# Optimization experiments

Hardware: AMD Instinct MI355X
Metric: run time of the kernel (lower is better)

Reference implementation:

```python
import jax, jax.numpy as jnp
import numpy as np

N_SI, N_M, N_INT, E = 100000, 100000, 500000, 500000
D_SI, D_M, D_INT, H1, H2 = 128, 128, 64, 32, 16


def _seg_mean(x_src, src, dst, n_dst):
    # gather src features per edge, scatter-mean into dst nodes
    msg = x_src[src]                                                  # [E, d]
    s = jax.ops.segment_sum(msg, dst, num_segments=n_dst)             # [n_dst, d]
    cnt = jax.ops.segment_sum(jnp.ones((src.shape[0],), x_src.dtype), dst,
                              num_segments=n_dst)
    return s / jnp.maximum(cnt, 1.0)[:, None]


def _sage(x_src, x_dst, src, dst, Wl, Wr, b):
    # PyG SAGEConv: lin_l(mean_aggr) + lin_r(x_dst); bias lives in lin_l
    return _seg_mean(x_src, src, dst, x_dst.shape[0]) @ Wl + b + x_dst @ Wr


def setup_inputs() -> dict:
    key = jax.random.key(0)
    ks = jax.random.split(key, 40)
    f = lambda i, shape: jax.random.normal(ks[i], shape, dtype=jnp.float32)
    w = lambda i, shape: 0.1 * jax.random.normal(ks[i], shape, dtype=jnp.float32)
    inp = {
        'x_si': f(0, (N_SI, D_SI)),
        'x_m': f(1, (N_M, D_M)),
        'x_int': f(2, (N_INT, D_INT)),
        # layer 1 SAGEConv params per relation (Wl: src->out, Wr: dst->out)
        'W1l_si2i': w(3, (D_SI, H1)), 'W1r_si2i': w(4, (D_INT, H1)), 'b1_si2i': w(5, (H1,)),
        'W1l_m2i': w(6, (D_M, H1)), 'W1r_m2i': w(7, (D_INT, H1)), 'b1_m2i': w(8, (H1,)),
        'W1l_si': w(9, (D_SI, H1)), 'W1r_si': w(10, (D_SI, H1)), 'b1_si': w(11, (H1,)),
        'W1l_m': w(12, (D_M, H1)), 'W1r_m': w(13, (D_M, H1)), 'b1_m': w(14, (H1,)),
        # layer 2
        'W2l_si2i': w(15, (H1, H2)), 'W2r_si2i': w(16, (H1, H2)), 'b2_si2i': w(17, (H2,)),
        'W2l_m2i': w(18, (H1, H2)), 'W2r_m2i': w(19, (H1, H2)), 'b2_m2i': w(20, (H2,)),
        'W2l_si': w(21, (H1, H2)), 'W2r_si': w(22, (H1, H2)), 'b2_si': w(23, (H2,)),
        'W2l_m': w(24, (H1, H2)), 'W2r_m': w(25, (H1, H2)), 'b2_m': w(26, (H2,)),
        # final linear
        'Wlin': w(27, (H2, 1)), 'blin': w(28, (1,)),
        # edge lists
        'src_si2i': jax.random.randint(ks[29], (E,), 0, N_SI, dtype=jnp.int32),
        'dst_si2i': jax.random.randint(ks[30], (E,), 0, N_INT, dtype=jnp.int32),
        'src_m2i': jax.random.randint(ks[31], (E,), 0, N_M, dtype=jnp.int32),
        'dst_m2i': jax.random.randint(ks[32], (E,), 0, N_INT, dtype=jnp.int32),
        'sl_si': jnp.arange(N_SI, dtype=jnp.int32),
        'sl_m': jnp.arange(N_M, dtype=jnp.int32),
    }
    return inp


def reference(x_si, x_m, x_int,
              W1l_si2i, W1r_si2i, b1_si2i, W1l_m2i, W1r_m2i, b1_m2i,
              W1l_si, W1r_si, b1_si, W1l_m, W1r_m, b1_m,
              W2l_si2i, W2r_si2i, b2_si2i, W2l_m2i, W2r_m2i, b2_m2i,
              W2l_si, W2r_si, b2_si, W2l_m, W2r_m, b2_m,
              Wlin, blin,
              src_si2i, dst_si2i, src_m2i, dst_m2i, sl_si, sl_m):
    # ---- HeteroConv layer 1 (aggr='mean' across relations per dst type) ----
    h_int = 0.5 * (_sage(x_si, x_int, src_si2i, dst_si2i, W1l_si2i, W1r_si2i, b1_si2i)
                   + _sage(x_m, x_int, src_m2i, dst_m2i, W1l_m2i, W1r_m2i, b1_m2i))
    h_si = _sage(x_si, x_si, sl_si, sl_si, W1l_si, W1r_si, b1_si)
    h_m = _sage(x_m, x_m, sl_m, sl_m, W1l_m, W1r_m, b1_m)
    # ReLU; dropout is identity in eval mode
    h_int, h_si, h_m = jax.nn.relu(h_int), jax.nn.relu(h_si), jax.nn.relu(h_m)
    # ---- HeteroConv layer 2 ----
    h_int2 = 0.5 * (_sage(h_si, h_int, src_si2i, dst_si2i, W2l_si2i, W2r_si2i, b2_si2i)
                    + _sage(h_m, h_int, src_m2i, dst_m2i, W2l_m2i, W2r_m2i, b2_m2i))
    # ---- readout on interaction nodes ----
    return (h_int2 @ Wlin + blin)[:, 0]
```

## Files before the change

kernel.cpp:

```cpp
#include <hip/hip_runtime.h>
#include <cstdint>

#define NSI   100000
#define NM    100000
#define NINT  500000
#define NEDGE 500000
#define NB_SCAN 489

static const long OFF_WSI  = 0;
static const long OFF_WM   = 8192;
static const long OFF_WI   = 16384;
static const long OFF_USI  = 18432;
static const long OFF_UM   = 18464;
static const long OFF_V    = 18496;
static const long OFF_C0   = 18528;
static const long OFF_BI   = 18560;
static const long OFF_PSI  = 18592;
static const long OFF_HSI  = OFF_PSI + 3200000;
static const long OFF_PM   = OFF_HSI + 3200000;
static const long OFF_HM   = OFF_PM + 3200000;
static const long OFF_SSI  = OFF_HM + 3200000;
static const long OFF_SM   = OFF_SSI + 100000;
static const long OFF_RI   = OFF_SM + 100000;
static const long OFF_DEG  = OFF_RI + 16000000;
static const long OFF_RP   = OFF_DEG + 2000000;
static const long OFF_EI   = OFF_RP + 1000000;
static const long OFF_BS   = OFF_EI + 1000000;
static const long OFF_END  = OFF_BS + 1024;

__global__ __launch_bounds__(256) void prep_kernel(
    const float* __restrict__ W1l_si2i, const float* __restrict__ W1l_si, const float* __restrict__ W1r_si,
    const float* __restrict__ W1l_m2i,  const float* __restrict__ W1l_m,  const float* __restrict__ W1r_m,
    const float* __restrict__ W1r_si2i, const float* __restrict__ W1r_m2i,
    const float* __restrict__ b1_si2i,  const float* __restrict__ b1_m2i,
    const float* __restrict__ W2l_si2i, const float* __restrict__ W2l_m2i,
    const float* __restrict__ W2r_si2i, const float* __restrict__ W2r_m2i,
    const float* __restrict__ b2_si2i,  const float* __restrict__ b2_m2i,
    const float* __restrict__ Wlin,     const float* __restrict__ blin,
    float* __restrict__ Wsi, float* __restrict__ Wm, float* __restrict__ Wi, float* __restrict__ bi,
    float* __restrict__ u_si, float* __restrict__ u_m, float* __restrict__ v, float* __restrict__ c0)
{
    const int tid = threadIdx.x;
    for (int idx = tid; idx < 128 * 64; idx += 256) {
        int k = idx >> 6, c = idx & 63;
        float a, b;
        if (c < 32) { a = W1l_si2i[k * 32 + c];      b = W1l_m2i[k * 32 + c]; }
        else { int cc = c - 32;
               a = W1l_si[k * 32 + cc] + W1r_si[k * 32 + cc];
               b = W1l_m[k * 32 + cc]  + W1r_m[k * 32 + cc]; }
        Wsi[idx] = a; Wm[idx] = b;
    }
    for (int idx = tid; idx < 64 * 32; idx += 256)
        Wi[idx] = 0.5f * (W1r_si2i[idx] + W1r_m2i[idx]);
    if (tid < 32) {
        bi[tid] = 0.5f * (b1_si2i[tid] + b1_m2i[tid]);
        float us = 0.f, um = 0.f, vv = 0.f;
        for (int k = 0; k < 16; ++k) {
            float wl = Wlin[k];
            us += W2l_si2i[tid * 16 + k] * wl;
            um += W2l_m2i[tid * 16 + k] * wl;
            vv += 0.5f * (W2r_si2i[tid * 16 + k] + W2r_m2i[tid * 16 + k]) * wl;
        }
        u_si[tid] = us; u_m[tid] = um; v[tid] = vv;
    }
    if (tid == 0) {
        float c = blin[0];
        for (int k = 0; k < 16; ++k) c += 0.5f * (b2_si2i[k] + b2_m2i[k]) * Wlin[k];
        c0[0] = c;
    }
}

__global__ __launch_bounds__(256) void gemm_src(
    const float* __restrict__ X, const float* __restrict__ Wcat, const float* __restrict__ bias,
    float* __restrict__ P, float* __restrict__ H, int N)
{
    __shared__ float xs[64 * 132];
    __shared__ float lw[64 * 64];
    const int tid = threadIdx.x;
    const long row_base = (long)blockIdx.x * 64;

    #pragma unroll
    for (int i = 0; i < 8; ++i) {
        int idx = tid + i * 256;
        int r = idx >> 5, k4 = idx & 31;
        long rr = row_base + r;
        float4 val = make_float4(0.f, 0.f, 0.f, 0.f);
        if (rr < N) val = ((const float4*)X)[rr * 32 + k4];
        *(float4*)&xs[r * 132 + k4 * 4] = val;
    }

    const int r0 = tid & 15;
    const int c0 = (tid >> 4) * 4;
    float acc[4][4] = {{0.f}};

    for (int half = 0; half < 2; ++half) {
        __syncthreads();
        #pragma unroll
        for (int i = 0; i < 4; ++i) {
            int idx = tid + i * 256;
            ((float4*)lw)[idx] = ((const float4*)Wcat)[half * 1024 + idx];
        }
        __syncthreads();
        const float* xb = xs + half * 64;
        #pragma unroll 4
        for (int k = 0; k < 64; k += 4) {
            float4 xr[4];
            #pragma unroll
            for (int j = 0; j < 4; ++j)
                xr[j] = *(const float4*)&xb[(r0 + 16 * j) * 132 + k];
            #pragma unroll
            for (int kk = 0; kk < 4; ++kk) {
                float4 wv = *(const float4*)&lw[(k + kk) * 64 + c0];
                #pragma unroll
                for (int j = 0; j < 4; ++j) {
                    float xv = (kk == 0) ? xr[j].x : (kk == 1) ? xr[j].y : (kk == 2) ? xr[j].z : xr[j].w;
                    acc[j][0] = fmaf(xv, wv.x, acc[j][0]);
                    acc[j][1] = fmaf(xv, wv.y, acc[j][1]);
                    acc[j][2] = fmaf(xv, wv.z, acc[j][2]);
                    acc[j][3] = fmaf(xv, wv.w, acc[j][3]);
                }
            }
        }
    }

    #pragma unroll
    for (int j = 0; j < 4; ++j) {
        long rr = row_base + r0 + 16 * j;
        if (rr >= N) continue;
        if (c0 < 32) {
            *(float4*)&P[rr * 32 + c0] = make_float4(acc[j][0], acc[j][1], acc[j][2], acc[j][3]);
        } else {
            const int cc = c0 - 32;
            float4 o;
            o.x = fmaxf(acc[j][0] + bias[cc + 0], 0.f);
            o.y = fmaxf(acc[j][1] + bias[cc + 1], 0.f);
            o.z = fmaxf(acc[j][2] + bias[cc + 2], 0.f);
            o.w = fmaxf(acc[j][3] + bias[cc + 3], 0.f);
            *(float4*)&H[rr * 32 + cc] = o;
        }
    }
}

__global__ __launch_bounds__(128) void gemm_int(
    const float* __restrict__ X, const float* __restrict__ W,
    const float* __restrict__ bi,
    float* __restrict__ R, int N)
{
    __shared__ float xs[64 * 68];
    __shared__ float lw[64 * 32];
    const int tid = threadIdx.x;
    const long row_base = (long)blockIdx.x * 64;

    #pragma unroll
    for (int i = 0; i < 4; ++i)
        ((float4*)lw)[tid + i * 128] = ((const float4*)W)[tid + i * 128];
    #pragma unroll
    for (int i = 0; i < 8; ++i) {
        int idx = tid + i * 128;
        int r = idx >> 4, k4 = idx & 15;
        long rr = row_base + r;
        float4 val = make_float4(0.f, 0.f, 0.f, 0.f);
        if (rr < N) val = ((const float4*)X)[rr * 16 + k4];
        *(float4*)&xs[r * 68 + k4 * 4] = val;
    }
    __syncthreads();

    const int r0 = tid & 15;
    const int c0 = (tid >> 4) * 4;
    float acc[4][4] = {{0.f}};
    #pragma unroll 4
    for (int k = 0; k < 64; k += 4) {
        float4 xr[4];
        #pragma unroll
        for (int j = 0; j < 4; ++j)
            xr[j] = *(const float4*)&xs[(r0 + 16 * j) * 68 + k];
        #pragma unroll
        for (int kk = 0; kk < 4; ++kk) {
            float4 wv = *(const float4*)&lw[(k + kk) * 32 + c0];
            #pragma unroll
            for (int j = 0; j < 4; ++j) {
                float xv = (kk == 0) ? xr[j].x : (kk == 1) ? xr[j].y : (kk == 2) ? xr[j].z : xr[j].w;
                acc[j][0] = fmaf(xv, wv.x, acc[j][0]);
                acc[j][1] = fmaf(xv, wv.y, acc[j][1]);
                acc[j][2] = fmaf(xv, wv.z, acc[j][2]);
                acc[j][3] = fmaf(xv, wv.w, acc[j][3]);
            }
        }
    }
    #pragma unroll
    for (int j = 0; j < 4; ++j) {
        long rr = row_base + r0 + 16 * j;
        if (rr >= N) continue;
        float4 o;
        o.x = acc[j][0] + bi[c0 + 0];
        o.y = acc[j][1] + bi[c0 + 1];
        o.z = acc[j][2] + bi[c0 + 2];
        o.w = acc[j][3] + bi[c0 + 3];
        *(float4*)&R[rr * 32 + c0] = o;
    }
}

__global__ __launch_bounds__(256) void s_kernel(
    const float* __restrict__ h_si, const float* __restrict__ h_m,
    const float* __restrict__ u_si, const float* __restrict__ u_m,
    float* __restrict__ s_si, float* __restrict__ s_m)
{
    long gid = (long)blockIdx.x * 256 + threadIdx.x;
    long node = gid >> 5;
    int f = (int)(gid & 31);
    if (node >= (long)(NSI + NM)) return;
    const float* h; const float* u; float* s; long n;
    if (node < NSI) { h = h_si; u = u_si; s = s_si; n = node; }
    else            { h = h_m;  u = u_m;  s = s_m;  n = node - NSI; }
    float t = h[n * 32 + f] * u[f];
    #pragma unroll
    for (int off = 16; off > 0; off >>= 1) t += __shfl_xor(t, off);
    if (f == 0) s[n] = t;
}

__global__ __launch_bounds__(256) void hist_kernel(
    const int* __restrict__ dst_si, const int* __restrict__ dst_m,
    int* __restrict__ deg_si, int* __restrict__ deg_m)
{
    int e = blockIdx.x * 256 + threadIdx.x;
    if (e >= NEDGE) return;
    if (blockIdx.y == 0) atomicAdd(&deg_si[dst_si[e]], 1);
    else                 atomicAdd(&deg_m[dst_m[e]], 1);
}

__global__ __launch_bounds__(256) void scan1_kernel(
    const int* __restrict__ deg_si, const int* __restrict__ deg_m,
    int* __restrict__ rp_si, int* __restrict__ rp_m, int* __restrict__ bsum)
{
    const int rel = blockIdx.y;
    const int* deg = rel ? deg_m : deg_si;
    int* rp = rel ? rp_m : rp_si;
    __shared__ int ls[256];
    const int tid = threadIdx.x;
    const int base = blockIdx.x * 1024 + tid * 4;
    int v[4];
    #pragma unroll
    for (int j = 0; j < 4; ++j) v[j] = (base + j < NINT) ? deg[base + j] : 0;
    int tsum = v[0] + v[1] + v[2] + v[3];
    ls[tid] = tsum;
    __syncthreads();
    for (int off = 1; off < 256; off <<= 1) {
        int t = (tid >= off) ? ls[tid - off] : 0;
        __syncthreads();
        ls[tid] += t;
        __syncthreads();
    }
    int run = ls[tid] - tsum;
    #pragma unroll
    for (int j = 0; j < 4; ++j) {
        if (base + j < NINT) rp[base + j] = run;
        run += v[j];
    }
    if (tid == 255) bsum[rel * 512 + blockIdx.x] = ls[255];
}

__global__ __launch_bounds__(512) void scan2_kernel(int* __restrict__ bsum)
{
    int* bs = bsum + blockIdx.y * 512;
    __shared__ int ls[512];
    const int tid = threadIdx.x;
    int v = (tid < NB_SCAN) ? bs[tid] : 0;
    ls[tid] = v;
    __syncthreads();
    for (int off = 1; off < 512; off <<= 1) {
        int t = (tid >= off) ? ls[tid - off] : 0;
        __syncthreads();
        ls[tid] += t;
        __syncthreads();
    }
    bs[tid] = ls[tid] - v;
}

__global__ __launch_bounds__(256) void scan3_kernel(
    int* __restrict__ rp_si, int* __restrict__ rp_m, const int* __restrict__ bsum)
{
    int i = blockIdx.x * 256 + threadIdx.x;
    if (i >= NINT) return;
    int rel = blockIdx.y;
    int* rp = rel ? rp_m : rp_si;
    rp[i] += bsum[rel * 512 + (i >> 10)];
}

__global__ __launch_bounds__(256) void fill_kernel(
    const int* __restrict__ src_si, const int* __restrict__ dst_si,
    const int* __restrict__ src_m,  const int* __restrict__ dst_m,
    const int* __restrict__ rp_si,  const int* __restrict__ rp_m,
    int* __restrict__ cur_si, int* __restrict__ cur_m,
    int* __restrict__ ei_si,  int* __restrict__ ei_m)
{
    int e = blockIdx.x * 256 + threadIdx.x;
    if (e >= NEDGE) return;
    if (blockIdx.y == 0) {
        int dn = dst_si[e], sn = src_si[e];
        int pos = atomicAdd(&cur_si[dn], 1);
        ei_si[rp_si[dn] + pos] = sn;
    } else {
        int dn = dst_m[e], sn = src_m[e];
        int pos = atomicAdd(&cur_m[dn], 1);
        ei_m[rp_m[dn] + pos] = sn;
    }
}

__global__ __launch_bounds__(256) void final_gather(
    const float* __restrict__ r_int,
    const float* __restrict__ p_si, const float* __restrict__ p_m,
    const float* __restrict__ s_si, const float* __restrict__ s_m,
    const int* __restrict__ rp_si, const int* __restrict__ deg_si, const int* __restrict__ ei_si,
    const int* __restrict__ rp_m,  const int* __restrict__ deg_m,  const int* __restrict__ ei_m,
    const float* __restrict__ v, const float* __restrict__ c0,
    float* __restrict__ out)
{
    long gid = (long)blockIdx.x * 256 + threadIdx.x;
    long node = gid >> 5;
    int f = (int)(gid & 31);
    if (node >= NINT) return;

    int ds = deg_si[node];
    int dm = deg_m[node];
    int rs = rp_si[node];
    int rm = rp_m[node];
    float r  = r_int[node * 32 + f];
    float vf = v[f];

    int sn_s = (ds > 0) ? ei_si[rs] : 0;
    int sn_m = (dm > 0) ? ei_m[rm] : 0;

    float ps = p_si[(long)sn_s * 32 + f];
    float pm = p_m[(long)sn_m * 32 + f];
    float qs = s_si[sn_s];
    float qm = s_m[sn_m];

    float a_si = (ds > 0) ? ps : 0.f;
    float a_m  = (dm > 0) ? pm : 0.f;
    float ss_si = (ds > 0) ? qs : 0.f;
    float ss_m  = (dm > 0) ? qm : 0.f;

    for (int e = 1; e < ds; ++e) {
        int sn = ei_si[rs + e];
        a_si  += p_si[(long)sn * 32 + f];
        ss_si += s_si[sn];
    }
    for (int e = 1; e < dm; ++e) {
        int sn = ei_m[rm + e];
        a_m  += p_m[(long)sn * 32 + f];
        ss_m += s_m[sn];
    }

    float csi = fmaxf((float)ds, 1.0f);
    float cm  = fmaxf((float)dm, 1.0f);

    float h = fmaxf(r + 0.5f * (a_si / csi + a_m / cm), 0.0f);
    float t = h * vf;
    #pragma unroll
    for (int off = 16; off > 0; off >>= 1) t += __shfl_xor(t, off);
    if (f == 0)
        out[node] = t + 0.5f * (ss_si / csi + ss_m / cm) + c0[0];
}

extern "C" void kernel_launch(void* const* d_in, const int* in_sizes, int n_in,
                              void* d_out, int out_size, void* d_ws, size_t ws_size,
                              hipStream_t stream)
{
    const float* x_si     = (const float*)d_in[0];
    const float* x_m      = (const float*)d_in[1];
    const float* x_int    = (const float*)d_in[2];
    const float* W1l_si2i = (const float*)d_in[3];
    const float* W1r_si2i = (const float*)d_in[4];
    const float* b1_si2i  = (const float*)d_in[5];
    const float* W1l_m2i  = (const float*)d_in[6];
    const float* W1r_m2i  = (const float*)d_in[7];
    const float* b1_m2i   = (const float*)d_in[8];
    const float* W1l_si   = (const float*)d_in[9];
    const float* W1r_si   = (const float*)d_in[10];
    const float* b1_si    = (const float*)d_in[11];
    const float* W1l_m    = (const float*)d_in[12];
    const float* W1r_m    = (const float*)d_in[13];
    const float* b1_m     = (const float*)d_in[14];
    const float* W2l_si2i = (const float*)d_in[15];
    const float* W2r_si2i = (const float*)d_in[16];
    const float* b2_si2i  = (const float*)d_in[17];
    const float* W2l_m2i  = (const float*)d_in[18];
    const float* W2r_m2i  = (const float*)d_in[19];
    const float* b2_m2i   = (const float*)d_in[20];
    const float* Wlin     = (const float*)d_in[27];
    const float* blin     = (const float*)d_in[28];
    const int* src_si2i   = (const int*)d_in[29];
    const int* dst_si2i   = (const int*)d_in[30];
    const int* src_m2i    = (const int*)d_in[31];
    const int* dst_m2i    = (const int*)d_in[32];

    float* ws = (float*)d_ws;
    if (ws_size < (size_t)OFF_END * sizeof(float)) return;

    int* deg_si = (int*)(ws + OFF_DEG);
    int* deg_m  = deg_si + 500000;
    int* cur_si = deg_si + 1000000;
    int* cur_m  = deg_si + 1500000;
    int* rp_si  = (int*)(ws + OFF_RP);
    int* rp_m   = rp_si + 500000;
    int* ei_si  = (int*)(ws + OFF_EI);
    int* ei_m   = ei_si + 500000;
    int* bsum   = (int*)(ws + OFF_BS);

    prep_kernel<<<1, 256, 0, stream>>>(
        W1l_si2i, W1l_si, W1r_si, W1l_m2i, W1l_m, W1r_m,
        W1r_si2i, W1r_m2i, b1_si2i, b1_m2i,
        W2l_si2i, W2l_m2i, W2r_si2i, W2r_m2i,
        b2_si2i, b2_m2i, Wlin, blin,
        ws + OFF_WSI, ws + OFF_WM, ws + OFF_WI, ws + OFF_BI,
        ws + OFF_USI, ws + OFF_UM, ws + OFF_V, ws + OFF_C0);

    hipMemsetAsync(deg_si, 0, 2000000 * sizeof(int), stream);

    dim3 egrid((NEDGE + 255) / 256, 2);
    hist_kernel<<<egrid, 256, 0, stream>>>(dst_si2i, dst_m2i, deg_si, deg_m);
    scan1_kernel<<<dim3(NB_SCAN, 2), 256, 0, stream>>>(deg_si, deg_m, rp_si, rp_m, bsum);
    scan2_kernel<<<dim3(1, 2), 512, 0, stream>>>(bsum);
    scan3_kernel<<<dim3((NINT + 255) / 256, 2), 256, 0, stream>>>(rp_si, rp_m, bsum);
    fill_kernel<<<egrid, 256, 0, stream>>>(src_si2i, dst_si2i, src_m2i, dst_m2i,
                                           rp_si, rp_m, cur_si, cur_m, ei_si, ei_m);

    gemm_src<<<(NSI + 63) / 64, 256, 0, stream>>>(x_si, ws + OFF_WSI, b1_si, ws + OFF_PSI, ws + OFF_HSI, NSI);
    gemm_src<<<(NM  + 63) / 64, 256, 0, stream>>>(x_m,  ws + OFF_WM,  b1_m,  ws + OFF_PM,  ws + OFF_HM,  NM);
    gemm_int<<<(NINT + 63) / 64, 128, 0, stream>>>(x_int, ws + OFF_WI, ws + OFF_BI, ws + OFF_RI, NINT);

    s_kernel<<<(NSI + NM) / 8, 256, 0, stream>>>(ws + OFF_HSI, ws + OFF_HM,
                                                 ws + OFF_USI, ws + OFF_UM,
                                                 ws + OFF_SSI, ws + OFF_SM);

    final_gather<<<NINT / 8, 256, 0, stream>>>(ws + OFF_RI,
                                               ws + OFF_PSI, ws + OFF_PM,
                                               ws + OFF_SSI, ws + OFF_SM,
                                               rp_si, deg_si, ei_si,
                                               rp_m,  deg_m,  ei_m,
                                               ws + OFF_V, ws + OFF_C0, (float*)d_out);
}
```

Baseline: 661.4 us.

## Fuse s-dot into source GEMM, vectorize final gather, reuse degree counters for fill

The layer-2 dot product with u is now computed inside the source GEMM epilogue through a shared-memory reduction, so the h_si/h_m buffers and the separate s_kernel are removed. The fill kernel counts down the degree array instead of using separate cursor arrays, which halves the memset, and the final gather reads degrees from row-pointer differences using a sentinel entry written in prep. The final gather uses 8 threads per node with float4 loads instead of 32 scalar threads. This cuts memory traffic and launches, but the atomic countdown consumes the degree array and makes the fill order reversed.

```diff
diff --git a/kernel.cpp b/kernel.cpp
--- a/kernel.cpp
+++ b/kernel.cpp
@@ -16,15 +16,13 @@
 static const long OFF_C0   = 18528;
 static const long OFF_BI   = 18560;
 static const long OFF_PSI  = 18592;
-static const long OFF_HSI  = OFF_PSI + 3200000;
-static const long OFF_PM   = OFF_HSI + 3200000;
-static const long OFF_HM   = OFF_PM + 3200000;
-static const long OFF_SSI  = OFF_HM + 3200000;
+static const long OFF_PM   = OFF_PSI + 3200000;
+static const long OFF_SSI  = OFF_PM + 3200000;
 static const long OFF_SM   = OFF_SSI + 100000;
 static const long OFF_RI   = OFF_SM + 100000;
 static const long OFF_DEG  = OFF_RI + 16000000;
-static const long OFF_RP   = OFF_DEG + 2000000;
-static const long OFF_EI   = OFF_RP + 1000000;
+static const long OFF_RP   = OFF_DEG + 1000000;
+static const long OFF_EI   = OFF_RP + 1000064;
 static const long OFF_BS   = OFF_EI + 1000000;
 static const long OFF_END  = OFF_BS + 1024;
 
@@ -38,7 +36,8 @@
     const float* __restrict__ b2_si2i,  const float* __restrict__ b2_m2i,
     const float* __restrict__ Wlin,     const float* __restrict__ blin,
     float* __restrict__ Wsi, float* __restrict__ Wm, float* __restrict__ Wi, float* __restrict__ bi,
-    float* __restrict__ u_si, float* __restrict__ u_m, float* __restrict__ v, float* __restrict__ c0)
+    float* __restrict__ u_si, float* __restrict__ u_m, float* __restrict__ v, float* __restrict__ c0,
+    int* __restrict__ rp_si, int* __restrict__ rp_m)
 {
     const int tid = threadIdx.x;
     for (int idx = tid; idx < 128 * 64; idx += 256) {
@@ -67,15 +66,19 @@
         float c = blin[0];
         for (int k = 0; k < 16; ++k) c += 0.5f * (b2_si2i[k] + b2_m2i[k]) * Wlin[k];
         c0[0] = c;
+        rp_si[NINT] = NEDGE;
+        rp_m[NINT]  = NEDGE;
     }
 }
 
 __global__ __launch_bounds__(256) void gemm_src(
     const float* __restrict__ X, const float* __restrict__ Wcat, const float* __restrict__ bias,
-    float* __restrict__ P, float* __restrict__ H, int N)
+    const float* __restrict__ u,
+    float* __restrict__ P, float* __restrict__ s_out, int N)
 {
     __shared__ float xs[64 * 132];
     __shared__ float lw[64 * 64];
+    __shared__ float sp[64 * 9];
     const int tid = threadIdx.x;
     const long row_base = (long)blockIdx.x * 64;
 
@@ -126,17 +129,27 @@
     #pragma unroll
     for (int j = 0; j < 4; ++j) {
         long rr = row_base + r0 + 16 * j;
-        if (rr >= N) continue;
         if (c0 < 32) {
-            *(float4*)&P[rr * 32 + c0] = make_float4(acc[j][0], acc[j][1], acc[j][2], acc[j][3]);
+            if (rr < N)
+                *(float4*)&P[rr * 32 + c0] = make_float4(acc[j][0], acc[j][1], acc[j][2], acc[j][3]);
         } else {
             const int cc = c0 - 32;
-            float4 o;
-            o.x = fmaxf(acc[j][0] + bias[cc + 0], 0.f);
-            o.y = fmaxf(acc[j][1] + bias[cc + 1], 0.f);
-            o.z = fmaxf(acc[j][2] + bias[cc + 2], 0.f);
-            o.w = fmaxf(acc[j][3] + bias[cc + 3], 0.f);
-            *(float4*)&H[rr * 32 + cc] = o;
+            float h0 = fmaxf(acc[j][0] + bias[cc + 0], 0.f);
+            float h1 = fmaxf(acc[j][1] + bias[cc + 1], 0.f);
+            float h2 = fmaxf(acc[j][2] + bias[cc + 2], 0.f);
+            float h3 = fmaxf(acc[j][3] + bias[cc + 3], 0.f);
+            float part = h0 * u[cc + 0] + h1 * u[cc + 1] + h2 * u[cc + 2] + h3 * u[cc + 3];
+            sp[(r0 + 16 * j) * 9 + (cc >> 2)] = part;
+        }
+    }
+    __syncthreads();
+    if (tid < 64) {
+        long rr = row_base + tid;
+        if (rr < N) {
+            float t = 0.f;
+            #pragma unroll
+            for (int g = 0; g < 8; ++g) t += sp[tid * 9 + g];
+            s_out[rr] = t;
         }
     }
 }
@@ -200,24 +213,6 @@
     }
 }
 
-__global__ __launch_bounds__(256) void s_kernel(
-    const float* __restrict__ h_si, const float* __restrict__ h_m,
-    const float* __restrict__ u_si, const float* __restrict__ u_m,
-    float* __restrict__ s_si, float* __restrict__ s_m)
-{
-    long gid = (long)blockIdx.x * 256 + threadIdx.x;
-    long node = gid >> 5;
-    int f = (int)(gid & 31);
-    if (node >= (long)(NSI + NM)) return;
-    const float* h; const float* u; float* s; long n;
-    if (node < NSI) { h = h_si; u = u_si; s = s_si; n = node; }
-    else            { h = h_m;  u = u_m;  s = s_m;  n = node - NSI; }
-    float t = h[n * 32 + f] * u[f];
-    #pragma unroll
-    for (int off = 16; off > 0; off >>= 1) t += __shfl_xor(t, off);
-    if (f == 0) s[n] = t;
-}
-
 __global__ __launch_bounds__(256) void hist_kernel(
     const int* __restrict__ dst_si, const int* __restrict__ dst_m,
     int* __restrict__ deg_si, int* __restrict__ deg_m)
@@ -290,19 +285,19 @@
     const int* __restrict__ src_si, const int* __restrict__ dst_si,
     const int* __restrict__ src_m,  const int* __restrict__ dst_m,
     const int* __restrict__ rp_si,  const int* __restrict__ rp_m,
-    int* __restrict__ cur_si, int* __restrict__ cur_m,
+    int* __restrict__ deg_si, int* __restrict__ deg_m,
     int* __restrict__ ei_si,  int* __restrict__ ei_m)
 {
     int e = blockIdx.x * 256 + threadIdx.x;
     if (e >= NEDGE) return;
     if (blockIdx.y == 0) {
         int dn = dst_si[e], sn = src_si[e];
-        int pos = atomicAdd(&cur_si[dn], 1);
-        ei_si[rp_si[dn] + pos] = sn;
+        int old = atomicSub(&deg_si[dn], 1);
+        ei_si[rp_si[dn] + old - 1] = sn;
     } else {
         int dn = dst_m[e], sn = src_m[e];
-        int pos = atomicAdd(&cur_m[dn], 1);
-        ei_m[rp_m[dn] + pos] = sn;
+        int old = atomicSub(&deg_m[dn], 1);
+        ei_m[rp_m[dn] + old - 1] = sn;
     }
 }
 
@@ -310,56 +305,63 @@
     const float* __restrict__ r_int,
     const float* __restrict__ p_si, const float* __restrict__ p_m,
     const float* __restrict__ s_si, const float* __restrict__ s_m,
-    const int* __restrict__ rp_si, const int* __restrict__ deg_si, const int* __restrict__ ei_si,
-    const int* __restrict__ rp_m,  const int* __restrict__ deg_m,  const int* __restrict__ ei_m,
+    const int* __restrict__ rp_si, const int* __restrict__ ei_si,
+    const int* __restrict__ rp_m,  const int* __restrict__ ei_m,
     const float* __restrict__ v, const float* __restrict__ c0,
     float* __restrict__ out)
 {
     long gid = (long)blockIdx.x * 256 + threadIdx.x;
-    long node = gid >> 5;
-    int f = (int)(gid & 31);
+    long node = gid >> 3;
+    int f4 = threadIdx.x & 7;
     if (node >= NINT) return;
 
-    int ds = deg_si[node];
-    int dm = deg_m[node];
-    int rs = rp_si[node];
-    int rm = rp_m[node];
-    float r  = r_int[node * 32 + f];
-    float vf = v[f];
+    int rs  = rp_si[node], res = rp_si[node + 1];
+    int rm  = rp_m[node],  rem = rp_m[node + 1];
+    float4 r  = ((const float4*)r_int)[node * 8 + f4];
+    float4 vf = ((const float4*)v)[f4];
+    int ds = res - rs, dm = rem - rm;
 
     int sn_s = (ds > 0) ? ei_si[rs] : 0;
     int sn_m = (dm > 0) ? ei_m[rm] : 0;
 
-    float ps = p_si[(long)sn_s * 32 + f];
-    float pm = p_m[(long)sn_m * 32 + f];
+    float4 ps = ((const float4*)p_si)[(long)sn_s * 8 + f4];
+    float4 pm = ((const float4*)p_m)[(long)sn_m * 8 + f4];
     float qs = s_si[sn_s];
     float qm = s_m[sn_m];
 
-    float a_si = (ds > 0) ? ps : 0.f;
-    float a_m  = (dm > 0) ? pm : 0.f;
-    float ss_si = (ds > 0) ? qs : 0.f;
-    float ss_m  = (dm > 0) ? qm : 0.f;
+    float msk_s = (ds > 0) ? 1.f : 0.f;
+    float msk_m = (dm > 0) ? 1.f : 0.f;
+    float4 a_si = make_float4(msk_s * ps.x, msk_s * ps.y, msk_s * ps.z, msk_s * ps.w);
+    float4 a_m  = make_float4(msk_m * pm.x, msk_m * pm.y, msk_m * pm.z, msk_m * pm.w);
+    float ss_si = msk_s * qs;
+    float ss_m  = msk_m * qm;
 
     for (int e = 1; e < ds; ++e) {
         int sn = ei_si[rs + e];
-        a_si  += p_si[(long)sn * 32 + f];
+        float4 p = ((const float4*)p_si)[(long)sn * 8 + f4];
+        a_si.x += p.x; a_si.y += p.y; a_si.z += p.z; a_si.w += p.w;
         ss_si += s_si[sn];
     }
     for (int e = 1; e < dm; ++e) {
         int sn = ei_m[rm + e];
-        a_m  += p_m[(long)sn * 32 + f];
+        float4 p = ((const float4*)p_m)[(long)sn * 8 + f4];
+        a_m.x += p.x; a_m.y += p.y; a_m.z += p.z; a_m.w += p.w;
         ss_m += s_m[sn];
     }
 
-    float csi = fmaxf((float)ds, 1.0f);
-    float cm  = fmaxf((float)dm, 1.0f);
-
-    float h = fmaxf(r + 0.5f * (a_si / csi + a_m / cm), 0.0f);
-    float t = h * vf;
-    #pragma unroll
-    for (int off = 16; off > 0; off >>= 1) t += __shfl_xor(t, off);
-    if (f == 0)
-        out[node] = t + 0.5f * (ss_si / csi + ss_m / cm) + c0[0];
+    float wsc = 0.5f / fmaxf((float)ds, 1.0f);
+    float wmc = 0.5f / fmaxf((float)dm, 1.0f);
+
+    float h0 = fmaxf(r.x + wsc * a_si.x + wmc * a_m.x, 0.f);
+    float h1 = fmaxf(r.y + wsc * a_si.y + wmc * a_m.y, 0.f);
+    float h2 = fmaxf(r.z + wsc * a_si.z + wmc * a_m.z, 0.f);
+    float h3 = fmaxf(r.w + wsc * a_si.w + wmc * a_m.w, 0.f);
+    float t = h0 * vf.x + h1 * vf.y + h2 * vf.z + h3 * vf.w;
+    t += __shfl_xor(t, 1);
+    t += __shfl_xor(t, 2);
+    t += __shfl_xor(t, 4);
+    if (f4 == 0)
+        out[node] = t + wsc * ss_si + wmc * ss_m + c0[0];
 }
 
 extern "C" void kernel_launch(void* const* d_in, const int* in_sizes, int n_in,
@@ -399,10 +401,8 @@
 
     int* deg_si = (int*)(ws + OFF_DEG);
     int* deg_m  = deg_si + 500000;
-    int* cur_si = deg_si + 1000000;
-    int* cur_m  = deg_si + 1500000;
     int* rp_si  = (int*)(ws + OFF_RP);
-    int* rp_m   = rp_si + 500000;
+    int* rp_m   = rp_si + 500032;
     int* ei_si  = (int*)(ws + OFF_EI);
     int* ei_m   = ei_si + 500000;
     int* bsum   = (int*)(ws + OFF_BS);
@@ -413,9 +413,10 @@
         W2l_si2i, W2l_m2i, W2r_si2i, W2r_m2i,
         b2_si2i, b2_m2i, Wlin, blin,
         ws + OFF_WSI, ws + OFF_WM, ws + OFF_WI, ws + OFF_BI,
-        ws + OFF_USI, ws + OFF_UM, ws + OFF_V, ws + OFF_C0);
-
-    hipMemsetAsync(deg_si, 0, 2000000 * sizeof(int), stream);
+        ws + OFF_USI, ws + OFF_UM, ws + OFF_V, ws + OFF_C0,
+        rp_si, rp_m);
+
+    hipMemsetAsync(deg_si, 0, 1000000 * sizeof(int), stream);
 
     dim3 egrid((NEDGE + 255) / 256, 2);
     hist_kernel<<<egrid, 256, 0, stream>>>(dst_si2i, dst_m2i, deg_si, deg_m);
@@ -423,20 +424,18 @@
     scan2_kernel<<<dim3(1, 2), 512, 0, stream>>>(bsum);
     scan3_kernel<<<dim3((NINT + 255) / 256, 2), 256, 0, stream>>>(rp_si, rp_m, bsum);
     fill_kernel<<<egrid, 256, 0, stream>>>(src_si2i, dst_si2i, src_m2i, dst_m2i,
-                                           rp_si, rp_m, cur_si, cur_m, ei_si, ei_m);
-
-    gemm_src<<<(NSI + 63) / 64, 256, 0, stream>>>(x_si, ws + OFF_WSI, b1_si, ws + OFF_PSI, ws + OFF_HSI, NSI);
-    gemm_src<<<(NM  + 63) / 64, 256, 0, stream>>>(x_m,  ws + OFF_WM,  b1_m,  ws + OFF_PM,  ws + OFF_HM,  NM);
+                                           rp_si, rp_m, deg_si, deg_m, ei_si, ei_m);
+
+    gemm_src<<<(NSI + 63) / 64, 256, 0, stream>>>(x_si, ws + OFF_WSI, b1_si, ws + OFF_USI,
+                                                  ws + OFF_PSI, ws + OFF_SSI, NSI);
+    gemm_src<<<(NM  + 63) / 64, 256, 0, stream>>>(x_m,  ws + OFF_WM,  b1_m,  ws + OFF_UM,
+                                                  ws + OFF_PM,  ws + OFF_SM,  NM);
     gemm_int<<<(NINT + 63) / 64, 128, 0, stream>>>(x_int, ws + OFF_WI, ws + OFF_BI, ws + OFF_RI, NINT);
 
-    s_kernel<<<(NSI + NM) / 8, 256, 0, stream>>>(ws + OFF_HSI, ws + OFF_HM,
-                                                 ws + OFF_USI, ws + OFF_UM,
-                                                 ws + OFF_SSI, ws + OFF_SM);
-
-    final_gather<<<NINT / 8, 256, 0, stream>>>(ws + OFF_RI,
-                                               ws + OFF_PSI, ws + OFF_PM,
-                                               ws + OFF_SSI, ws + OFF_SM,
-                                               rp_si, deg_si, ei_si,
-                                               rp_m,  deg_m,  ei_m,
-                                               ws + OFF_V, ws + OFF_C0, (float*)d_out);
-}
+    final_gather<<<(NINT * 8) / 256, 256, 0, stream>>>(ws + OFF_RI,
+                                                       ws + OFF_PSI, ws + OFF_PM,
+                                                       ws + OFF_SSI, ws + OFF_SM,
+                                                       rp_si, ei_si,
+                                                       rp_m,  ei_m,
+                                                       ws + OFF_V, ws + OFF_C0, (float*)d_out);
+}
```

Result: faster. 593.2 us (-10.3%).
